# Kernel optimization log

Measured on AMD Instinct MI355X. Metric: run time of the kernel, lower is better.

Reference implementation:

```python
import jax, jax.numpy as jnp
import numpy as np

NUM_LEVELS = 16
FEAT = 2
LOG2_HASH = 19
HASH_SIZE = 1 << LOG2_HASH          # 524288 entries per level
BASE_RES = 16
FINEST_RES = 512
BBOX_MIN, BBOX_MAX = -1.0, 1.0
N_POINTS = 1 << 21                  # ~2M query positions

# per-level grid resolutions (instant-NGP geometric progression)
RESOLUTIONS = [int(np.floor(BASE_RES * np.exp(i * np.log(FINEST_RES / BASE_RES) / (NUM_LEVELS - 1))))
               for i in range(NUM_LEVELS)]

# 8 voxel corner offsets, order matches the torch module
_OFFSETS = jnp.array([[0, 0, 0], [0, 0, 1], [0, 1, 0], [0, 1, 1],
                      [1, 0, 0], [1, 0, 1], [1, 1, 0], [1, 1, 1]], dtype=jnp.float32)
# spatial-hash primes (uint32 wraparound preserves the low 19 bits used by mod 2^19,
# so results match torch's int64 arithmetic exactly)
_PRIMES = jnp.array([1, 2654435761, 805459861], dtype=jnp.uint32)
_MASK = jnp.uint32(HASH_SIZE - 1)


def setup_inputs() -> dict:
    key = jax.random.key(0)
    k1, k2 = jax.random.split(key)
    positions = jax.random.uniform(k1, (N_POINTS, 3), jnp.float32, BBOX_MIN, BBOX_MAX)
    # hash tables initialized uniform(-1e-4, 1e-4) as in the torch module
    tables = jax.random.uniform(k2, (NUM_LEVELS, HASH_SIZE, FEAT), jnp.float32, -1e-4, 1e-4)
    return {"positions": positions, "tables": tables}


def _encode_level(positions, table, resolution):
    # positions: [N,3] in [BBOX_MIN, BBOX_MAX]; table: [HASH_SIZE, FEAT]
    normalized = (positions - BBOX_MIN) / (BBOX_MAX - BBOX_MIN)   # [N,3] in [0,1]
    scaled = normalized * resolution
    floor = jnp.floor(scaled)
    frac = scaled - floor                                         # [N,3]
    corners = jnp.clip(floor[:, None, :] + _OFFSETS[None, :, :], 0.0, resolution)  # [N,8,3]
    c = corners.astype(jnp.uint32)
    hashed = (c[..., 0] * _PRIMES[0]) ^ (c[..., 1] * _PRIMES[1]) ^ (c[..., 2] * _PRIMES[2])
    idx = (hashed & _MASK).astype(jnp.int32)                      # [N,8]
    # trilinear weights: prod over dims of (frac if offset==1 else 1-frac)
    w = jnp.prod(jnp.where(_OFFSETS[None] > 0.5, frac[:, None, :], 1.0 - frac[:, None, :]),
                 axis=-1)                                          # [N,8]
    feats = table[idx]                                            # [N,8,FEAT] gather
    return jnp.einsum('ncf,nc->nf', feats, w)                     # [N,FEAT]


def reference(positions, tables):
    # returns [N, NUM_LEVELS * FEAT], levels concatenated along feature dim
    outs = [_encode_level(positions, tables[l], float(RESOLUTIONS[l]))
            for l in range(NUM_LEVELS)]
    return jnp.concatenate(outs, axis=-1)
```

## Files before the change

### kernel.cpp

```cpp
#include <hip/hip_runtime.h>
#include <hip/hip_fp16.h>
#include <stdint.h>
#include <cmath>

static constexpr int NUM_LEVELS = 16;
static constexpr uint32_t HASH_SIZE = 1u << 19;
static constexpr uint32_t HMASK = HASH_SIZE - 1u;
static constexpr int NB = 32;
static constexpr int NBUCKETS = NB * NB * NB;
static constexpr int CAP = 128;
static constexpr int OVCAP = 8192;

typedef float    f2_t __attribute__((ext_vector_type(2)));
typedef float    f4_t __attribute__((ext_vector_type(4)));
typedef uint32_t u4_t __attribute__((ext_vector_type(4)));

struct ResArr { float r[NUM_LEVELS]; };

__device__ __forceinline__ void make_corners(
    float px, float py, float pz, float res, uint32_t* idx, float* w)
{
    float sx = ((px + 1.0f) * 0.5f) * res;
    float sy = ((py + 1.0f) * 0.5f) * res;
    float sz = ((pz + 1.0f) * 0.5f) * res;

    float fx = floorf(sx), fy = floorf(sy), fz = floorf(sz);
    float rx = sx - fx, ry = sy - fy, rz = sz - fz;

    float x0f = fminf(fmaxf(fx, 0.f), res), x1f = fminf(fmaxf(fx + 1.f, 0.f), res);
    float y0f = fminf(fmaxf(fy, 0.f), res), y1f = fminf(fmaxf(fy + 1.f, 0.f), res);
    float z0f = fminf(fmaxf(fz, 0.f), res), z1f = fminf(fmaxf(fz + 1.f, 0.f), res);

    uint32_t x0 = (uint32_t)x0f, x1 = (uint32_t)x1f;
    uint32_t hy0 = (uint32_t)y0f * 2654435761u, hy1 = (uint32_t)y1f * 2654435761u;
    uint32_t hz0 = (uint32_t)z0f * 805459861u,  hz1 = (uint32_t)z1f * 805459861u;

    float wx0 = 1.f - rx, wx1 = rx;
    float wy0 = 1.f - ry, wy1 = ry;
    float wz0 = 1.f - rz, wz1 = rz;

    idx[0] = (x0 ^ hy0 ^ hz0) & HMASK; w[0] = (wx0 * wy0) * wz0;
    idx[1] = (x0 ^ hy0 ^ hz1) & HMASK; w[1] = (wx0 * wy0) * wz1;
    idx[2] = (x0 ^ hy1 ^ hz0) & HMASK; w[2] = (wx0 * wy1) * wz0;
    idx[3] = (x0 ^ hy1 ^ hz1) & HMASK; w[3] = (wx0 * wy1) * wz1;
    idx[4] = (x1 ^ hy0 ^ hz0) & HMASK; w[4] = (wx1 * wy0) * wz0;
    idx[5] = (x1 ^ hy0 ^ hz1) & HMASK; w[5] = (wx1 * wy0) * wz1;
    idx[6] = (x1 ^ hy1 ^ hz0) & HMASK; w[6] = (wx1 * wy1) * wz0;
    idx[7] = (x1 ^ hy1 ^ hz1) & HMASK; w[7] = (wx1 * wy1) * wz1;
}

__device__ __forceinline__ void enc_all16(
    float px, float py, float pz, const uint32_t* __restrict__ tbl16,
    const ResArr& ra, f4_t r[8])
{
    #pragma unroll
    for (int p = 0; p < 8; ++p) {
        const uint32_t* tA = tbl16 + (size_t)(2 * p)     * HASH_SIZE;
        const uint32_t* tB = tbl16 + (size_t)(2 * p + 1) * HASH_SIZE;
        uint32_t idxA[8], idxB[8];
        float wA[8], wB[8];
        make_corners(px, py, pz, ra.r[2 * p],     idxA, wA);
        make_corners(px, py, pz, ra.r[2 * p + 1], idxB, wB);

        uint32_t g[16];
        #pragma unroll
        for (int i = 0; i < 8; ++i) g[i]     = tA[idxA[i]];
        #pragma unroll
        for (int i = 0; i < 8; ++i) g[8 + i] = tB[idxB[i]];

        float a0 = 0.f, a1 = 0.f, b0 = 0.f, b1 = 0.f;
        #pragma unroll
        for (int i = 0; i < 8; ++i) {
            union { uint32_t u; __half2 h2; } c; c.u = g[i];
            float2 f = __half22float2(c.h2);
            a0 += wA[i] * f.x; a1 += wA[i] * f.y;
        }
        #pragma unroll
        for (int i = 0; i < 8; ++i) {
            union { uint32_t u; __half2 h2; } c; c.u = g[8 + i];
            float2 f = __half22float2(c.h2);
            b0 += wB[i] * f.x; b1 += wB[i] * f.y;
        }
        r[p] = (f4_t){a0, a1, b0, b1};
    }
}

__global__ __launch_bounds__(256) void convert_kernel8(
    const f4_t* __restrict__ tables4, uint32_t* __restrict__ tbl16, int nthreads)
{
    int t = blockIdx.x * 256 + threadIdx.x;
    if (t >= nthreads) return;
    const f4_t* src = tables4 + (size_t)t * 4;
    f4_t v0 = __builtin_nontemporal_load(src + 0);
    f4_t v1 = __builtin_nontemporal_load(src + 1);
    f4_t v2 = __builtin_nontemporal_load(src + 2);
    f4_t v3 = __builtin_nontemporal_load(src + 3);
    union { __half2 h2; uint32_t u; } c0, c1, c2, c3, c4, c5, c6, c7;
    c0.h2 = __floats2half2_rn(v0.x, v0.y); c1.h2 = __floats2half2_rn(v0.z, v0.w);
    c2.h2 = __floats2half2_rn(v1.x, v1.y); c3.h2 = __floats2half2_rn(v1.z, v1.w);
    c4.h2 = __floats2half2_rn(v2.x, v2.y); c5.h2 = __floats2half2_rn(v2.z, v2.w);
    c6.h2 = __floats2half2_rn(v3.x, v3.y); c7.h2 = __floats2half2_rn(v3.z, v3.w);
    u4_t o0 = {c0.u, c1.u, c2.u, c3.u};
    u4_t o1 = {c4.u, c5.u, c6.u, c7.u};
    u4_t* dst = reinterpret_cast<u4_t*>(tbl16) + (size_t)t * 2;
    __builtin_nontemporal_store(o0, dst + 0);
    __builtin_nontemporal_store(o1, dst + 1);
}

__global__ __launch_bounds__(256) void scatter4_kernel(
    const f4_t* __restrict__ pos4, f4_t* __restrict__ padded,
    uint32_t* __restrict__ counts, uint32_t* __restrict__ ovcnt,
    f4_t* __restrict__ ovlist, int nquads)
{
    int q = blockIdx.x * 256 + threadIdx.x;
    if (q >= nquads) return;
    f4_t a = __builtin_nontemporal_load(pos4 + (size_t)q * 3 + 0);
    f4_t b = __builtin_nontemporal_load(pos4 + (size_t)q * 3 + 1);
    f4_t c = __builtin_nontemporal_load(pos4 + (size_t)q * 3 + 2);
    float xs[4] = {a.x, a.w, b.z, c.y};
    float ys[4] = {a.y, b.x, b.w, c.z};
    float zs[4] = {a.z, b.y, c.x, c.w};
    #pragma unroll
    for (int j = 0; j < 4; ++j) {
        int kx = min(max((int)((xs[j] + 1.f) * 16.f), 0), NB - 1);
        int ky = min(max((int)((ys[j] + 1.f) * 16.f), 0), NB - 1);
        int kz = min(max((int)((zs[j] + 1.f) * 16.f), 0), NB - 1);
        int bucket = (kx << 10) | (ky << 5) | kz;
        uint32_t rank = atomicAdd(&counts[bucket], 1u);
        f4_t rec = {xs[j], ys[j], zs[j], __uint_as_float((uint32_t)(q * 4 + j))};
        if (rank < (uint32_t)CAP) {
            padded[(size_t)bucket * CAP + rank] = rec;
        } else {
            uint32_t ov = atomicAdd(ovcnt, 1u);
            if (ov < (uint32_t)OVCAP) ovlist[ov] = rec;
        }
    }
}

__global__ __launch_bounds__(256) void hashenc_padded_kernel(
    const f4_t* __restrict__ padded, const uint32_t* __restrict__ counts,
    const uint32_t* __restrict__ tbl16, float* __restrict__ out,
    int nchunk, ResArr ra)
{
    int bid = blockIdx.x;
    int sbid = (bid & 7) * nchunk + (bid >> 3);
    int gid = sbid * 256 + threadIdx.x;
    int bucket = gid >> 7;
    int slot   = gid & (CAP - 1);
    uint32_t cnt = counts[bucket];
    if (slot >= (int)min(cnt, (uint32_t)CAP)) return;

    f4_t t = padded[gid];
    float px = t.x, py = t.y, pz = t.z;
    uint32_t orig = __float_as_uint(t.w);

    f4_t r[8];
    enc_all16(px, py, pz, tbl16, ra, r);

    f4_t* dst = reinterpret_cast<f4_t*>(out + (size_t)orig * 32);
    #pragma unroll
    for (int k = 0; k < 8; ++k) dst[k] = r[k];
}

__global__ __launch_bounds__(256) void overflow_kernel(
    const f4_t* __restrict__ ovlist, const uint32_t* __restrict__ ovcnt,
    const uint32_t* __restrict__ tbl16, float* __restrict__ out, ResArr ra)
{
    uint32_t n = min(*ovcnt, (uint32_t)OVCAP);
    for (uint32_t i = threadIdx.x; i < n; i += 256) {
        f4_t t = ovlist[i];
        f4_t r[8];
        enc_all16(t.x, t.y, t.z, tbl16, ra, r);
        f4_t* dst = reinterpret_cast<f4_t*>(out + (size_t)__float_as_uint(t.w) * 32);
        #pragma unroll
        for (int k = 0; k < 8; ++k) dst[k] = r[k];
    }
}

__global__ __launch_bounds__(256) void convert_kernel(
    const f2_t* __restrict__ tables, uint32_t* __restrict__ out, int total)
{
    int i = blockIdx.x * 256 + threadIdx.x;
    if (i >= total) return;
    f2_t v = __builtin_nontemporal_load(&tables[i]);
    __half2 h = __floats2half2_rn(v.x, v.y);
    union { __half2 h2; uint32_t u; } cvt; cvt.h2 = h;
    __builtin_nontemporal_store(cvt.u, &out[i]);
}

__global__ __launch_bounds__(256) void hist_kernel(
    const float* __restrict__ pos, uint32_t* __restrict__ counts, int n)
{
    int i = blockIdx.x * 256 + threadIdx.x;
    if (i >= n) return;
    int kx = min(max((int)((pos[(size_t)i*3+0] + 1.f) * 16.f), 0), NB - 1);
    int ky = min(max((int)((pos[(size_t)i*3+1] + 1.f) * 16.f), 0), NB - 1);
    int kz = min(max((int)((pos[(size_t)i*3+2] + 1.f) * 16.f), 0), NB - 1);
    atomicAdd(&counts[(kx << 10) | (ky << 5) | kz], 1u);
}

__global__ __launch_bounds__(1024) void scan_kernel(
    const uint32_t* __restrict__ counts, uint32_t* __restrict__ offsets)
{
    __shared__ uint32_t lds[1024];
    int tid = threadIdx.x;
    uint32_t running = 0;
    for (int chunk = 0; chunk < NBUCKETS; chunk += 1024) {
        uint32_t v = counts[chunk + tid];
        lds[tid] = v;
        __syncthreads();
        #pragma unroll
        for (int off = 1; off < 1024; off <<= 1) {
            uint32_t t = (tid >= off) ? lds[tid - off] : 0u;
            __syncthreads();
            lds[tid] += t;
            __syncthreads();
        }
        offsets[chunk + tid] = running + lds[tid] - v;
        running += lds[1023];
        __syncthreads();
    }
}

__global__ __launch_bounds__(256) void scatter_kernel(
    const float* __restrict__ pos, uint32_t* __restrict__ offs,
    float4* __restrict__ sorted, int n)
{
    int i = blockIdx.x * 256 + threadIdx.x;
    if (i >= n) return;
    float px = pos[(size_t)i*3+0], py = pos[(size_t)i*3+1], pz = pos[(size_t)i*3+2];
    int kx = min(max((int)((px + 1.f) * 16.f), 0), NB - 1);
    int ky = min(max((int)((py + 1.f) * 16.f), 0), NB - 1);
    int kz = min(max((int)((pz + 1.f) * 16.f), 0), NB - 1);
    uint32_t slot = atomicAdd(&offs[(kx << 10) | (ky << 5) | kz], 1u);
    sorted[slot] = make_float4(px, py, pz, __uint_as_float((uint32_t)i));
}

__global__ __launch_bounds__(256) void hashenc_sorted_kernel(
    const float4* __restrict__ sorted, const uint32_t* __restrict__ tbl16,
    float* __restrict__ out, int n_points, int nchunk, ResArr ra)
{
    int bid = blockIdx.x;
    int sbid = (bid & 7) * nchunk + (bid >> 3);
    int gid = sbid * 256 + threadIdx.x;
    if (gid >= n_points) return;
    f4_t t = __builtin_nontemporal_load(reinterpret_cast<const f4_t*>(sorted) + gid);
    f4_t r[8];
    enc_all16(t.x, t.y, t.z, tbl16, ra, r);
    f4_t* dst = reinterpret_cast<f4_t*>(out + (size_t)__float_as_uint(t.w) * 32);
    #pragma unroll
    for (int k = 0; k < 8; ++k) dst[k] = r[k];
}

__global__ __launch_bounds__(256) void hashenc_fp32_kernel(
    const float* __restrict__ pos, const float* __restrict__ tables,
    float* __restrict__ out, int n_points, ResArr res_arr)
{
    int tid = blockIdx.x * 256 + threadIdx.x;
    if (tid >= n_points * NUM_LEVELS) return;
    int level = tid & (NUM_LEVELS - 1);
    int point = tid >> 4;
    float px = pos[(size_t)point*3+0], py = pos[(size_t)point*3+1], pz = pos[(size_t)point*3+2];
    uint32_t idx[8]; float w[8];
    make_corners(px, py, pz, res_arr.r[level], idx, w);
    const float2* tbl = reinterpret_cast<const float2*>(tables) + (size_t)level * HASH_SIZE;
    float acc0 = 0.f, acc1 = 0.f;
    #pragma unroll
    for (int i = 0; i < 8; ++i) {
        float2 f = tbl[idx[i]];
        acc0 += w[i] * f.x; acc1 += w[i] * f.y;
    }
    union { float acc[2]; double d; } u;
    u.acc[0] = acc0; u.acc[1] = acc1;
    __builtin_nontemporal_store(u.d, reinterpret_cast<double*>(out) + ((size_t)point * 16 + level));
}

extern "C" void kernel_launch(void* const* d_in, const int* in_sizes, int n_in,
                              void* d_out, int out_size, void* d_ws, size_t ws_size,
                              hipStream_t stream) {
    const float* pos    = (const float*)d_in[0];
    const float* tables = (const float*)d_in[1];
    float* out = (float*)d_out;
    int n_points = in_sizes[0] / 3;

    ResArr ra;
    const double log32 = log(32.0);
    for (int i = 0; i < NUM_LEVELS; ++i)
        ra.r[i] = (float)(int)floor(16.0 * exp(((double)i * log32) / 15.0));

    const size_t tbl_bytes = (size_t)NUM_LEVELS * HASH_SIZE * sizeof(uint32_t);
    const size_t pad_bytes = (size_t)NBUCKETS * CAP * sizeof(f4_t);
    const size_t cnt_bytes = (size_t)NBUCKETS * sizeof(uint32_t);
    const size_t ov_bytes  = 16 + (size_t)OVCAP * sizeof(f4_t);
    const size_t need_pad  = tbl_bytes + pad_bytes + cnt_bytes + ov_bytes;

    const size_t sorted_bytes = (size_t)n_points * sizeof(float4);
    const size_t need_sorted  = tbl_bytes + sorted_bytes + 2 * cnt_bytes;

    int pblocks = (n_points + 255) / 256;
    int ttotal  = NUM_LEVELS * (int)HASH_SIZE;

    if (ws_size >= need_pad && n_points <= (1 << 21) && (n_points & 3) == 0) {
        char* ws = (char*)d_ws;
        uint32_t* tbl16  = (uint32_t*)(ws);
        f4_t*     padded = (f4_t*)(ws + tbl_bytes);
        uint32_t* counts = (uint32_t*)(ws + tbl_bytes + pad_bytes);
        uint32_t* ovcnt  = (uint32_t*)(ws + tbl_bytes + pad_bytes + cnt_bytes);
        f4_t*     ovlist = (f4_t*)(ws + tbl_bytes + pad_bytes + cnt_bytes + 16);

        hipMemsetAsync(counts, 0, cnt_bytes + 16, stream);
        int cthreads = ttotal / 8;
        convert_kernel8<<<(cthreads + 255) / 256, 256, 0, stream>>>(
            (const f4_t*)tables, tbl16, cthreads);
        int nquads = n_points / 4;
        scatter4_kernel<<<(nquads + 255) / 256, 256, 0, stream>>>(
            (const f4_t*)pos, padded, counts, ovcnt, ovlist, nquads);

        int nblocks = NBUCKETS * CAP / 256;
        int nchunk  = nblocks / 8;
        hashenc_padded_kernel<<<nblocks, 256, 0, stream>>>(
            padded, counts, tbl16, out, nchunk, ra);
        overflow_kernel<<<1, 256, 0, stream>>>(ovlist, ovcnt, tbl16, out, ra);
    } else if (ws_size >= need_sorted) {
        char* ws = (char*)d_ws;
        uint32_t* tbl16   = (uint32_t*)(ws);
        float4*   sorted  = (float4*)(ws + tbl_bytes);
        uint32_t* offsets = (uint32_t*)(ws + tbl_bytes + sorted_bytes);
        uint32_t* counts  = (uint32_t*)(ws + tbl_bytes + sorted_bytes + cnt_bytes);

        convert_kernel<<<(ttotal + 255) / 256, 256, 0, stream>>>(
            (const f2_t*)tables, tbl16, ttotal);
        hipMemsetAsync(counts, 0, cnt_bytes, stream);
        hist_kernel<<<pblocks, 256, 0, stream>>>(pos, counts, n_points);
        scan_kernel<<<1, 1024, 0, stream>>>(counts, offsets);
        scatter_kernel<<<pblocks, 256, 0, stream>>>(pos, offsets, sorted, n_points);
        int nchunk = (pblocks + 7) / 8;
        hashenc_sorted_kernel<<<nchunk * 8, 256, 0, stream>>>(
            sorted, tbl16, out, n_points, nchunk, ra);
    } else {
        long long total = (long long)n_points * NUM_LEVELS;
        hashenc_fp32_kernel<<<(int)((total + 255) / 256), 256, 0, stream>>>(
            pos, tables, out, n_points, ra);
    }
}
```

Baseline: 632.1 us.

## Stage coarse-level hash table neighborhoods in LDS per spatial bucket pair

For the 10 coarsest levels, each block first gathers every hash-table entry its two spatial buckets can touch into shared memory, then has points interpolate from LDS instead of issuing scattered global gathers. The finer 6 levels still gather from global memory. This is meant to cut redundant global gather traffic and latency for coarse levels where many points share corners. The cost is extra staging loads (about 3k entries per block, some never used), a barrier, and LDS use that may lower occupancy.

After: 678.0 us. +7.3%, slower.

```diff
diff --git a/kernel.cpp b/kernel.cpp
--- a/kernel.cpp
+++ b/kernel.cpp
@@ -11,42 +11,60 @@
 static constexpr int CAP = 128;
 static constexpr int OVCAP = 8192;
 
+static constexpr int NSTAGED = 10;
+__device__ __constant__ const int SW[NSTAGED]   = {4,4,4,4,5,5,5,6,7,7};
+__device__ __constant__ const int SOFF[NSTAGED] = {0,64,128,192,256,381,506,631,847,1190};
+static constexpr int STOT = 1533;
+
 typedef float    f2_t __attribute__((ext_vector_type(2)));
 typedef float    f4_t __attribute__((ext_vector_type(4)));
 typedef uint32_t u4_t __attribute__((ext_vector_type(4)));
 
 struct ResArr { float r[NUM_LEVELS]; };
 
-__device__ __forceinline__ void make_corners(
-    float px, float py, float pz, float res, uint32_t* idx, float* w)
+__device__ __forceinline__ void corner_setup(
+    float px, float py, float pz, float res,
+    int xi[2], int yi[2], int zi[2], float wx[2], float wy[2], float wz[2])
 {
     float sx = ((px + 1.0f) * 0.5f) * res;
     float sy = ((py + 1.0f) * 0.5f) * res;
     float sz = ((pz + 1.0f) * 0.5f) * res;
-
     float fx = floorf(sx), fy = floorf(sy), fz = floorf(sz);
     float rx = sx - fx, ry = sy - fy, rz = sz - fz;
-
-    float x0f = fminf(fmaxf(fx, 0.f), res), x1f = fminf(fmaxf(fx + 1.f, 0.f), res);
-    float y0f = fminf(fmaxf(fy, 0.f), res), y1f = fminf(fmaxf(fy + 1.f, 0.f), res);
-    float z0f = fminf(fmaxf(fz, 0.f), res), z1f = fminf(fmaxf(fz + 1.f, 0.f), res);
-
-    uint32_t x0 = (uint32_t)x0f, x1 = (uint32_t)x1f;
-    uint32_t hy0 = (uint32_t)y0f * 2654435761u, hy1 = (uint32_t)y1f * 2654435761u;
-    uint32_t hz0 = (uint32_t)z0f * 805459861u,  hz1 = (uint32_t)z1f * 805459861u;
-
-    float wx0 = 1.f - rx, wx1 = rx;
-    float wy0 = 1.f - ry, wy1 = ry;
-    float wz0 = 1.f - rz, wz1 = rz;
-
-    idx[0] = (x0 ^ hy0 ^ hz0) & HMASK; w[0] = (wx0 * wy0) * wz0;
-    idx[1] = (x0 ^ hy0 ^ hz1) & HMASK; w[1] = (wx0 * wy0) * wz1;
-    idx[2] = (x0 ^ hy1 ^ hz0) & HMASK; w[2] = (wx0 * wy1) * wz0;
-    idx[3] = (x0 ^ hy1 ^ hz1) & HMASK; w[3] = (wx0 * wy1) * wz1;
-    idx[4] = (x1 ^ hy0 ^ hz0) & HMASK; w[4] = (wx1 * wy0) * wz0;
-    idx[5] = (x1 ^ hy0 ^ hz1) & HMASK; w[5] = (wx1 * wy0) * wz1;
-    idx[6] = (x1 ^ hy1 ^ hz0) & HMASK; w[6] = (wx1 * wy1) * wz0;
-    idx[7] = (x1 ^ hy1 ^ hz1) & HMASK; w[7] = (wx1 * wy1) * wz1;
+    xi[0] = (int)fminf(fmaxf(fx, 0.f), res);       xi[1] = (int)fminf(fmaxf(fx + 1.f, 0.f), res);
+    yi[0] = (int)fminf(fmaxf(fy, 0.f), res);       yi[1] = (int)fminf(fmaxf(fy + 1.f, 0.f), res);
+    zi[0] = (int)fminf(fmaxf(fz, 0.f), res);       zi[1] = (int)fminf(fmaxf(fz + 1.f, 0.f), res);
+    wx[0] = 1.f - rx; wx[1] = rx;
+    wy[0] = 1.f - ry; wy[1] = ry;
+    wz[0] = 1.f - rz; wz[1] = rz;
+}
+
+__device__ __forceinline__ void enc_level_global(
+    float px, float py, float pz, float res, const uint32_t* __restrict__ tbl,
+    float& o0, float& o1)
+{
+    int xi[2], yi[2], zi[2]; float wx[2], wy[2], wz[2];
+    corner_setup(px, py, pz, res, xi, yi, zi, wx, wy, wz);
+    uint32_t hy0 = (uint32_t)yi[0] * 2654435761u, hy1 = (uint32_t)yi[1] * 2654435761u;
+    uint32_t hz0 = (uint32_t)zi[0] * 805459861u,  hz1 = (uint32_t)zi[1] * 805459861u;
+    uint32_t g[8];
+    g[0] = tbl[((uint32_t)xi[0] ^ hy0 ^ hz0) & HMASK];
+    g[1] = tbl[((uint32_t)xi[0] ^ hy0 ^ hz1) & HMASK];
+    g[2] = tbl[((uint32_t)xi[0] ^ hy1 ^ hz0) & HMASK];
+    g[3] = tbl[((uint32_t)xi[0] ^ hy1 ^ hz1) & HMASK];
+    g[4] = tbl[((uint32_t)xi[1] ^ hy0 ^ hz0) & HMASK];
+    g[5] = tbl[((uint32_t)xi[1] ^ hy0 ^ hz1) & HMASK];
+    g[6] = tbl[((uint32_t)xi[1] ^ hy1 ^ hz0) & HMASK];
+    g[7] = tbl[((uint32_t)xi[1] ^ hy1 ^ hz1) & HMASK];
+    float a0 = 0.f, a1 = 0.f;
+    #pragma unroll
+    for (int c = 0; c < 8; ++c) {
+        union { uint32_t u; __half2 h2; } cv; cv.u = g[c];
+        float2 f = __half22float2(cv.h2);
+        float w = (wx[c >> 2] * wy[(c >> 1) & 1]) * wz[c & 1];
+        a0 += w * f.x; a1 += w * f.y;
+    }
+    o0 = a0; o1 = a1;
 }
 
 __device__ __forceinline__ void enc_all16(
@@ -55,32 +73,9 @@
 {
     #pragma unroll
     for (int p = 0; p < 8; ++p) {
-        const uint32_t* tA = tbl16 + (size_t)(2 * p)     * HASH_SIZE;
-        const uint32_t* tB = tbl16 + (size_t)(2 * p + 1) * HASH_SIZE;
-        uint32_t idxA[8], idxB[8];
-        float wA[8], wB[8];
-        make_corners(px, py, pz, ra.r[2 * p],     idxA, wA);
-        make_corners(px, py, pz, ra.r[2 * p + 1], idxB, wB);
-
-        uint32_t g[16];
-        #pragma unroll
-        for (int i = 0; i < 8; ++i) g[i]     = tA[idxA[i]];
-        #pragma unroll
-        for (int i = 0; i < 8; ++i) g[8 + i] = tB[idxB[i]];
-
-        float a0 = 0.f, a1 = 0.f, b0 = 0.f, b1 = 0.f;
-        #pragma unroll
-        for (int i = 0; i < 8; ++i) {
-            union { uint32_t u; __half2 h2; } c; c.u = g[i];
-            float2 f = __half22float2(c.h2);
-            a0 += wA[i] * f.x; a1 += wA[i] * f.y;
-        }
-        #pragma unroll
-        for (int i = 0; i < 8; ++i) {
-            union { uint32_t u; __half2 h2; } c; c.u = g[8 + i];
-            float2 f = __half22float2(c.h2);
-            b0 += wB[i] * f.x; b1 += wB[i] * f.y;
-        }
+        float a0, a1, b0, b1;
+        enc_level_global(px, py, pz, ra.r[2*p],   tbl16 + (size_t)(2*p)   * HASH_SIZE, a0, a1);
+        enc_level_global(px, py, pz, ra.r[2*p+1], tbl16 + (size_t)(2*p+1) * HASH_SIZE, b0, b1);
         r[p] = (f4_t){a0, a1, b0, b1};
     }
 }
@@ -137,25 +132,92 @@
     }
 }
 
-__global__ __launch_bounds__(256) void hashenc_padded_kernel(
+__global__ __launch_bounds__(256) void hashenc_lds_kernel(
     const f4_t* __restrict__ padded, const uint32_t* __restrict__ counts,
     const uint32_t* __restrict__ tbl16, float* __restrict__ out,
     int nchunk, ResArr ra)
 {
+    __shared__ uint32_t slds[2][STOT];
+
     int bid = blockIdx.x;
     int sbid = (bid & 7) * nchunk + (bid >> 3);
-    int gid = sbid * 256 + threadIdx.x;
+    int tid = threadIdx.x;
+    int bkt0 = sbid << 1;
+
+    for (int e = tid; e < 2 * STOT; e += 256) {
+        int lb  = (e >= STOT) ? 1 : 0;
+        int idx = e - lb * STOT;
+        int bucket = bkt0 + lb;
+        int kx = bucket >> 10, ky = (bucket >> 5) & 31, kz = bucket & 31;
+        int lvl, lx, ly, lz, W;
+        if (idx < 256)      { lvl = idx >> 6; int loc = idx & 63;  W = 4; lz = loc & 3; ly = (loc >> 2) & 3; lx = loc >> 4; }
+        else if (idx < 631) { int t = idx - 256; lvl = 4 + t / 125; int loc = t - (lvl - 4) * 125; W = 5; lz = loc % 5; int t2 = loc / 5; ly = t2 % 5; lx = t2 / 5; }
+        else if (idx < 847) { lvl = 7; int loc = idx - 631; W = 6; lz = loc % 6; int t2 = loc / 6; ly = t2 % 6; lx = t2 / 6; }
+        else                { int t = idx - 847; lvl = 8 + t / 343; int loc = t - (lvl - 8) * 343; W = 7; lz = loc % 7; int t2 = loc / 7; ly = t2 % 7; lx = t2 / 7; }
+        float R = ra.r[lvl];
+        int bx = (int)floorf((float)kx * R * 0.03125f) - 1;
+        int by = (int)floorf((float)ky * R * 0.03125f) - 1;
+        int bz = (int)floorf((float)kz * R * 0.03125f) - 1;
+        uint32_t gx = (uint32_t)(bx + lx), gy = (uint32_t)(by + ly), gz = (uint32_t)(bz + lz);
+        uint32_t h = gx ^ (gy * 2654435761u) ^ (gz * 805459861u);
+        slds[lb][idx] = tbl16[(size_t)lvl * HASH_SIZE + (h & HMASK)];
+    }
+    __syncthreads();
+
+    int gid = sbid * 256 + tid;
     int bucket = gid >> 7;
     int slot   = gid & (CAP - 1);
+    int lb     = tid >> 7;
     uint32_t cnt = counts[bucket];
     if (slot >= (int)min(cnt, (uint32_t)CAP)) return;
 
     f4_t t = padded[gid];
     float px = t.x, py = t.y, pz = t.z;
     uint32_t orig = __float_as_uint(t.w);
+    int kx = bucket >> 10, ky = (bucket >> 5) & 31, kz = bucket & 31;
+    const uint32_t* sb = slds[lb];
 
     f4_t r[8];
-    enc_all16(px, py, pz, tbl16, ra, r);
+    #pragma unroll
+    for (int p = 0; p < 5; ++p) {
+        float acc[4];
+        #pragma unroll
+        for (int h2 = 0; h2 < 2; ++h2) {
+            const int lvl = 2 * p + h2;
+            const int W   = SW[lvl];
+            const int off = SOFF[lvl];
+            float R = ra.r[lvl];
+            int bx = (int)floorf((float)kx * R * 0.03125f) - 1;
+            int by = (int)floorf((float)ky * R * 0.03125f) - 1;
+            int bz = (int)floorf((float)kz * R * 0.03125f) - 1;
+            int xi[2], yi[2], zi[2]; float wx[2], wy[2], wz[2];
+            corner_setup(px, py, pz, R, xi, yi, zi, wx, wy, wz);
+            int lx0 = xi[0] - bx, lx1 = xi[1] - bx;
+            int ly0 = yi[0] - by, ly1 = yi[1] - by;
+            int lz0 = zi[0] - bz, lz1 = zi[1] - bz;
+            float a0 = 0.f, a1 = 0.f;
+            #pragma unroll
+            for (int c = 0; c < 8; ++c) {
+                int lx = (c & 4) ? lx1 : lx0;
+                int ly = (c & 2) ? ly1 : ly0;
+                int lz = (c & 1) ? lz1 : lz0;
+                union { uint32_t u; __half2 hh; } cv;
+                cv.u = sb[off + (lx * W + ly) * W + lz];
+                float2 f = __half22float2(cv.hh);
+                float w = (wx[c >> 2] * wy[(c >> 1) & 1]) * wz[c & 1];
+                a0 += w * f.x; a1 += w * f.y;
+            }
+            acc[2 * h2] = a0; acc[2 * h2 + 1] = a1;
+        }
+        r[p] = (f4_t){acc[0], acc[1], acc[2], acc[3]};
+    }
+    #pragma unroll
+    for (int p = 5; p < 8; ++p) {
+        float a0, a1, b0, b1;
+        enc_level_global(px, py, pz, ra.r[2*p],   tbl16 + (size_t)(2*p)   * HASH_SIZE, a0, a1);
+        enc_level_global(px, py, pz, ra.r[2*p+1], tbl16 + (size_t)(2*p+1) * HASH_SIZE, b0, b1);
+        r[p] = (f4_t){a0, a1, b0, b1};
+    }
 
     f4_t* dst = reinterpret_cast<f4_t*>(out + (size_t)orig * 32);
     #pragma unroll
@@ -261,14 +323,21 @@
     int level = tid & (NUM_LEVELS - 1);
     int point = tid >> 4;
     float px = pos[(size_t)point*3+0], py = pos[(size_t)point*3+1], pz = pos[(size_t)point*3+2];
-    uint32_t idx[8]; float w[8];
-    make_corners(px, py, pz, res_arr.r[level], idx, w);
+    float res = res_arr.r[level];
+    int xi[2], yi[2], zi[2]; float wx[2], wy[2], wz[2];
+    corner_setup(px, py, pz, res, xi, yi, zi, wx, wy, wz);
+    uint32_t hy0 = (uint32_t)yi[0] * 2654435761u, hy1 = (uint32_t)yi[1] * 2654435761u;
+    uint32_t hz0 = (uint32_t)zi[0] * 805459861u,  hz1 = (uint32_t)zi[1] * 805459861u;
     const float2* tbl = reinterpret_cast<const float2*>(tables) + (size_t)level * HASH_SIZE;
     float acc0 = 0.f, acc1 = 0.f;
     #pragma unroll
-    for (int i = 0; i < 8; ++i) {
-        float2 f = tbl[idx[i]];
-        acc0 += w[i] * f.x; acc1 += w[i] * f.y;
+    for (int c = 0; c < 8; ++c) {
+        uint32_t hx = (uint32_t)xi[c >> 2];
+        uint32_t hy = (c & 2) ? hy1 : hy0;
+        uint32_t hz = (c & 1) ? hz1 : hz0;
+        float2 f = tbl[(hx ^ hy ^ hz) & HMASK];
+        float w = (wx[c >> 2] * wy[(c >> 1) & 1]) * wz[c & 1];
+        acc0 += w * f.x; acc1 += w * f.y;
     }
     union { float acc[2]; double d; } u;
     u.acc[0] = acc0; u.acc[1] = acc1;
@@ -318,7 +387,7 @@
 
         int nblocks = NBUCKETS * CAP / 256;
         int nchunk  = nblocks / 8;
-        hashenc_padded_kernel<<<nblocks, 256, 0, stream>>>(
+        hashenc_lds_kernel<<<nblocks, 256, 0, stream>>>(
             padded, counts, tbl16, out, nchunk, ra);
         overflow_kernel<<<1, 256, 0, stream>>>(ovlist, ovcnt, tbl16, out, ra);
     } else if (ws_size >= need_sorted) {
```
